# Optimization experiments

Measured on AMD Instinct MI355X. Metric: run time of the kernel, lower is better.

Reference implementation:

```python
import jax, jax.numpy as jnp
import numpy as np

B, S, N, C = 128, 512, 64, 1
F = N * C          # flattened feature dim = input_size * n_nodes
H = 512            # hidden_size


def _gru_imputer(x2d, m2d, Wih, Whh, bih, bhh, Wro, bro):
    """Unidirectional 1-step-ahead GRU imputer.
    x2d: [B,S,F] float, m2d: [B,S,F] bool.
    Returns (x_hat [B,S,F], h [B,S,H])."""
    dt = x2d.dtype
    h0 = jnp.zeros((x2d.shape[0], H), dtype=dt)
    xhat0 = h0 @ Wro.T + bro  # readout of initial state (== bro)

    def step(carry, inp):
        h, xhat = carry
        x_t, m_t = inp  # [B,F] float, [B,F] bool
        x_p = jnp.where(m_t, x_t, xhat)
        x_in = jnp.concatenate([x_p, m_t.astype(dt)], axis=-1)  # [B,2F]
        gi = x_in @ Wih.T + bih  # [B,3H]
        gh = h @ Whh.T + bhh     # [B,3H]
        ir, iz, inn = jnp.split(gi, 3, axis=-1)
        hr, hz, hn = jnp.split(gh, 3, axis=-1)
        r = jax.nn.sigmoid(ir + hr)
        z = jax.nn.sigmoid(iz + hz)
        n = jnp.tanh(inn + r * hn)
        h_new = (1.0 - z) * n + z * h
        xhat_new = h_new @ Wro.T + bro
        return (h_new, xhat_new), (h_new, xhat_new)

    xs = (jnp.swapaxes(x2d[:, :-1], 0, 1), jnp.swapaxes(m2d[:, :-1], 0, 1))
    _, (hs, xhats) = jax.lax.scan(step, (h0, xhat0), xs)
    hs = jnp.concatenate([h0[None], hs], axis=0)        # [S,B,H]
    xhats = jnp.concatenate([xhat0[None], xhats], axis=0)  # [S,B,F]
    return jnp.swapaxes(xhats, 0, 1), jnp.swapaxes(hs, 0, 1)


def setup_inputs() -> dict:
    key = jax.random.key(0)
    ks = jax.random.split(key, 16)
    s = 1.0 / np.sqrt(H)
    u = lambda k, shape: jax.random.uniform(k, shape, jnp.float32, -s, s)
    inp = {
        "x": jax.random.normal(ks[0], (B, S, N, C), jnp.float32),
        "mask": jax.random.randint(ks[1], (B, S, N, C), 0, 2).astype(bool),
        # forward-direction RNN params
        "Wih_f": u(ks[2], (3 * H, 2 * F)),
        "Whh_f": u(ks[3], (3 * H, H)),
        "bih_f": u(ks[4], (3 * H,)),
        "bhh_f": u(ks[5], (3 * H,)),
        "Wro_f": u(ks[6], (F, H)),
        "bro_f": u(ks[7], (F,)),
        # backward-direction RNN params
        "Wih_b": u(ks[8], (3 * H, 2 * F)),
        "Whh_b": u(ks[9], (3 * H, H)),
        "bih_b": u(ks[10], (3 * H,)),
        "bhh_b": u(ks[11], (3 * H,)),
        "Wro_b": u(ks[12], (F, H)),
        "bro_b": u(ks[13], (F,)),
        # final bidirectional readout
        "Wout": u(ks[14], (F, 2 * H)),
        "bout": u(ks[15], (F,)),
    }
    return inp


def reference(x, mask, Wih_f, Whh_f, bih_f, bhh_f, Wro_f, bro_f,
              Wih_b, Whh_b, bih_b, bhh_b, Wro_b, bro_b, Wout, bout):
    # rearrange 'b s n c -> b s (n c)'
    x2d = x.reshape(B, S, F)
    m2d = mask.reshape(B, S, F)

    xh_f, h_f = _gru_imputer(x2d, m2d, Wih_f, Whh_f, bih_f, bhh_f, Wro_f, bro_f)
    xh_b, h_b = _gru_imputer(x2d[:, ::-1], m2d[:, ::-1],
                             Wih_b, Whh_b, bih_b, bhh_b, Wro_b, bro_b)
    xh_b = xh_b[:, ::-1]
    h_b = h_b[:, ::-1]

    h = jnp.concatenate([h_f, h_b], axis=-1)  # [B,S,2H]; dropout p=0 -> identity
    x_hat = (h @ Wout.T + bout).reshape(B, S, N, C)
    return (x_hat, xh_f.reshape(B, S, N, C), xh_b.reshape(B, S, N, C))
```

## Files before the change

kernel.cpp:

```cpp
#include <hip/hip_runtime.h>

#define Bx 128
#define Sx 512
#define Fx 64
#define Hx 512
#define Xx 128

#define PARTB_OFF 0ull
#define H_OFF     ((size_t)Bx * Sx * Fx)
#define XHB_OFF   (H_OFF + (size_t)2 * 2 * Hx * Bx)
#define BAR_OFF   (XHB_OFF + (size_t)4 * 2 * Bx * Fx)
#define FLAG_OFF  (BAR_OFF + 4096)

#define LDSW_WHH   0
#define LDSW_XIN   26112
#define LDSW_WRO   (LDSW_XIN + 32 * 160)
#define LDSW_WOUT  (LDSW_WRO + 2 * 544)
#define LDSW_WROS  (LDSW_WOUT + 2 * 544)
#define LDSW_HX    (LDSW_WROS + 1088)
#define LDSW_TOTAL (LDSW_HX + 512 + 16)

struct BParams {
  const float* x; const void* mask;
  const float* Wih_f; const float* Whh_f; const float* bih_f; const float* bhh_f;
  const float* Wro_f; const float* bro_f;
  const float* Wih_b; const float* Whh_b; const float* bih_b; const float* bhh_b;
  const float* Wro_b; const float* bro_b;
  const float* Wout; const float* bout;
  float* out; float* ws;
};

__global__ void detect_kernel(const unsigned int* mask, float* ws) {
  int* bars = (int*)(ws + BAR_OFF);
  int* flag = (int*)(ws + FLAG_OFF);
  int t = threadIdx.x;
  for (int i = t; i < 4096; i += blockDim.x) bars[i] = 0;
  if (t == 0) *flag = 0;
  __syncthreads();
  unsigned int v = 0;
  for (int i = t; i < 4096; i += blockDim.x) v |= mask[i] & 0xFFFFFF00u;
  if (v) atomicOr(flag, 1);
}

__global__ void combine_kernel(float* out, const float* partb, const float* bout) {
  int i = blockIdx.x * blockDim.x + threadIdx.x;
  out[i] = out[i] + partb[i] + bout[i & 63];
}

__device__ __forceinline__ float sel8(const float* a, int idx) {
  float v = a[0];
#pragma unroll
  for (int i = 1; i < 8; ++i) v = (idx == i) ? a[i] : v;
  return v;
}

__device__ __forceinline__ void st_sys(float* p, float v) {
  __hip_atomic_store(p, v, __ATOMIC_RELAXED, __HIP_MEMORY_SCOPE_SYSTEM);
}
__device__ __forceinline__ void st_sys_i(int* p, int v) {
  __hip_atomic_store(p, v, __ATOMIC_RELAXED, __HIP_MEMORY_SCOPE_SYSTEM);
}

__device__ __forceinline__ void gbar(int* slots, int hs, int nbar) {
  __syncthreads();
  if (threadIdx.x < 64) {
    if (threadIdx.x == 0) st_sys_i(slots + hs * 16, nbar);
    const int* myslot = slots + (threadIdx.x & 31) * 16;
    for (;;) {
      int v = __hip_atomic_load(myslot, __ATOMIC_RELAXED, __HIP_MEMORY_SCOPE_AGENT);
      if (__all(v >= nbar)) break;
      __builtin_amdgcn_s_sleep(1);
    }
    asm volatile("buffer_inv\n\ts_waitcnt vmcnt(0)" ::: "memory");
  }
  __syncthreads();
}

#define GH_STEP(C, JOFF) {                                                   \
  const float* hr = hrd + (size_t)(j0 + jj + (JOFF)) * Bx + bA;              \
  float4 ha  = *(const float4*)(hr);                                         \
  float4 hbv = *(const float4*)(hr + 4);                                     \
  float s0 = w0.C, s1 = w1.C, s2 = w2.C;                                     \
  acc0[0]=fmaf(s0,ha.x,acc0[0]);  acc0[1]=fmaf(s0,ha.y,acc0[1]);             \
  acc0[2]=fmaf(s0,ha.z,acc0[2]);  acc0[3]=fmaf(s0,ha.w,acc0[3]);             \
  acc0[4]=fmaf(s0,hbv.x,acc0[4]); acc0[5]=fmaf(s0,hbv.y,acc0[5]);            \
  acc0[6]=fmaf(s0,hbv.z,acc0[6]); acc0[7]=fmaf(s0,hbv.w,acc0[7]);            \
  acc1[0]=fmaf(s1,ha.x,acc1[0]);  acc1[1]=fmaf(s1,ha.y,acc1[1]);             \
  acc1[2]=fmaf(s1,ha.z,acc1[2]);  acc1[3]=fmaf(s1,ha.w,acc1[3]);             \
  acc1[4]=fmaf(s1,hbv.x,acc1[4]); acc1[5]=fmaf(s1,hbv.y,acc1[5]);            \
  acc1[6]=fmaf(s1,hbv.z,acc1[6]); acc1[7]=fmaf(s1,hbv.w,acc1[7]);            \
  acc3[0]=fmaf(s2,ha.x,acc3[0]);  acc3[1]=fmaf(s2,ha.y,acc3[1]);             \
  acc3[2]=fmaf(s2,ha.z,acc3[2]);  acc3[3]=fmaf(s2,ha.w,acc3[3]);             \
  acc3[4]=fmaf(s2,hbv.x,acc3[4]); acc3[5]=fmaf(s2,hbv.y,acc3[5]);            \
  acc3[6]=fmaf(s2,hbv.z,acc3[6]); acc3[7]=fmaf(s2,hbv.w,acc3[7]); }

__global__ void __launch_bounds__(512, 2)
birnn_main(BParams p) {
  extern __shared__ float lds[];

  const int w   = blockIdx.x;
  const int g   = w & 7;
  const int dir = g >> 2;
  const int bg  = g & 3;
  const int hs  = w >> 3;
  const int b0  = bg * 32;
  const int u0  = hs * 16;
  const int f0  = hs * 2;
  const int tid = threadIdx.x;

  const float* Wih = dir ? p.Wih_b : p.Wih_f;
  const float* Whh = dir ? p.Whh_b : p.Whh_f;
  const float* bih = dir ? p.bih_b : p.bih_f;
  const float* bhh = dir ? p.bhh_b : p.bhh_f;
  const float* Wro = dir ? p.Wro_b : p.Wro_f;
  const float* bro = dir ? p.bro_b : p.bro_f;

  float* hbuf  = p.ws + H_OFF;
  float* xhb4  = p.ws + XHB_OFF;
  int*   slots = (int*)(p.ws + BAR_OFF) + g * 512;
  const int u8f = *(const int*)(p.ws + FLAG_OFF);
  const unsigned char* m8  = (const unsigned char*)p.mask;
  const int*           m32 = (const int*)p.mask;

  float* pout   = dir ? (p.ws + PARTB_OFF) : p.out;
  float* out_xh = p.out + (size_t)(1 + dir) * Bx * Sx * Fx;

  for (int idx = tid; idx < 3 * 16 * 512; idx += 512) {
    int g3 = idx >> 13; int rem = idx & 8191;
    int u = rem >> 9;   int j = rem & 511;
    lds[LDSW_WHH + ((g3 * 16 + u) * 8 + (j >> 6)) * 68 + (j & 63)] =
        Whh[(size_t)(g3 * 512 + u0 + u) * Hx + j];
  }
  for (int idx = tid; idx < 2 * 512; idx += 512) {
    int f = idx >> 9, j = idx & 511;
    lds[LDSW_WRO  + f * 544 + (j >> 6) * 68 + (j & 63)] = Wro[(size_t)(f0 + f) * Hx + j];
    lds[LDSW_WOUT + f * 544 + (j >> 6) * 68 + (j & 63)] =
        p.Wout[(size_t)(f0 + f) * (2 * Hx) + dir * Hx + j];
  }
  for (int idx = tid; idx < 64 * 16; idx += 512) {
    int f = idx >> 4, u = idx & 15;
    lds[LDSW_WROS + f * 17 + u] = Wro[(size_t)f * Hx + u0 + u];
  }

  if (hs == 0) {
    for (int idx = tid; idx < 32 * 512; idx += 512) {
      int u = idx >> 5, bo = idx & 31;
      st_sys(&hbuf[((size_t)(dir * 2 + 0) * Hx + u) * Bx + b0 + bo], 0.f);
    }
  }
  float bro_own = 0.f;
  if (tid < 64) {
    bro_own = bro[tid];
#pragma unroll
    for (int q = 0; q < 4; ++q)
      st_sys(&xhb4[(((size_t)q * 2 + dir) * Bx + (b0 + hs)) * Fx + tid], bro_own);
  }

  const int jq   = tid & 7;
  const int ulo  = (tid >> 3) & 7;
  const int wv   = tid >> 6;
  const int bsub = wv & 3;
  const int uhi  = wv >> 2;
  const int u    = uhi * 8 + ulo;
  const int bA   = b0 + bsub * 8;
  const int ru   = u0 + u;
  const int j0   = jq * 64;
  const int blo  = (tid >> 3) & 7;
  const int bB   = b0 + (wv & 3) * 8 + blo;
  const int fB   = wv >> 2;
  const int pf   = tid & 63;
  const int pbq  = tid >> 6;

  float4 wih0[4], wih1[4], wih2[4];
#pragma unroll
  for (int q = 0; q < 4; ++q) {
    wih0[q] = *(const float4*)(Wih + (size_t)(0 * 512 + ru) * Xx + jq * 16 + q * 4);
    wih1[q] = *(const float4*)(Wih + (size_t)(1 * 512 + ru) * Xx + jq * 16 + q * 4);
    wih2[q] = *(const float4*)(Wih + (size_t)(2 * 512 + ru) * Xx + jq * 16 + q * 4);
  }
  const float bs_r = bih[ru] + bhh[ru];
  const float bs_z = bih[512 + ru] + bhh[512 + ru];
  const float bs_i = bih[1024 + ru];
  const float bs_h = bhh[1024 + ru];

  const float* w0p = lds + LDSW_WHH + ((0 * 16 + u) * 8 + jq) * 68;
  const float* w1p = lds + LDSW_WHH + ((1 * 16 + u) * 8 + jq) * 68;
  const float* w2p = lds + LDSW_WHH + ((2 * 16 + u) * 8 + jq) * 68;

  float hprev_own = 0.f;

  int nbar = 1;
  gbar(slots, hs, nbar);

  for (int k = 1; k < Sx; ++k) {
    const int pp = k & 1, pr = pp ^ 1;
    const int t_in = dir ? (Sx - k) : (k - 1);
    const int rdq = (k - 1) & 3;
    const int adq = k & 3;
    const int inq = (k + 2) & 3;

    {
      int bl = tid >> 4, sub = tid & 15;
      int b = b0 + bl;
      float* xr = lds + LDSW_XIN + bl * 160 + (sub >> 1) * 20 + (sub & 1) * 8;
      float v[8];
      if (sub < 8) {
        size_t base = ((size_t)b * Sx + t_in) * Fx + sub * 8;
        float4 xa = *(const float4*)(p.x + base);
        float4 xb = *(const float4*)(p.x + base + 4);
        const float* xhp = xhb4 + (((size_t)rdq * 2 + dir) * Bx + b) * Fx + sub * 8;
        float4 ha  = *(const float4*)(xhp);
        float4 hb4 = *(const float4*)(xhp + 4);
        int mi[8];
        if (u8f) {
          unsigned long long mm = *(const unsigned long long*)(m8 + base);
#pragma unroll
          for (int j = 0; j < 8; ++j) mi[j] = (int)((mm >> (8 * j)) & 0xFF);
        } else {
          int4 ma = *(const int4*)(m32 + base);
          int4 mb = *(const int4*)(m32 + base + 4);
          mi[0] = ma.x; mi[1] = ma.y; mi[2] = ma.z; mi[3] = ma.w;
          mi[4] = mb.x; mi[5] = mb.y; mi[6] = mb.z; mi[7] = mb.w;
        }
        v[0] = mi[0] ? xa.x : ha.x;  v[1] = mi[1] ? xa.y : ha.y;
        v[2] = mi[2] ? xa.z : ha.z;  v[3] = mi[3] ? xa.w : ha.w;
        v[4] = mi[4] ? xb.x : hb4.x; v[5] = mi[5] ? xb.y : hb4.y;
        v[6] = mi[6] ? xb.z : hb4.z; v[7] = mi[7] ? xb.w : hb4.w;
      } else {
        size_t base = ((size_t)b * Sx + t_in) * Fx + (sub - 8) * 8;
        if (u8f) {
          unsigned long long mm = *(const unsigned long long*)(m8 + base);
#pragma unroll
          for (int j = 0; j < 8; ++j) v[j] = (float)((mm >> (8 * j)) & 0xFF);
        } else {
          int4 ma = *(const int4*)(m32 + base);
          int4 mb = *(const int4*)(m32 + base + 4);
          v[0] = (float)ma.x; v[1] = (float)ma.y; v[2] = (float)ma.z; v[3] = (float)ma.w;
          v[4] = (float)mb.x; v[5] = (float)mb.y; v[6] = (float)mb.z; v[7] = (float)mb.w;
        }
      }
      *(float4*)(xr)     = make_float4(v[0], v[1], v[2], v[3]);
      *(float4*)(xr + 4) = make_float4(v[4], v[5], v[6], v[7]);
    }
    if (tid < 64) {
      float v = xhb4[(((size_t)rdq * 2 + dir) * Bx + (b0 + hs)) * Fx + tid];
      st_sys(&out_xh[((size_t)(b0 + hs) * Sx + t_in) * Fx + tid], v);
    }
    {
      const float* hnw  = hbuf + (size_t)(dir * 2 + pr) * Hx * Bx;
      const float* wouL = lds + LDSW_WOUT + fB * 544 + jq * 68;
      const float* hcol = hnw + (size_t)j0 * Bx + bB;
      float ap = 0.f;
#pragma unroll 4
      for (int jj = 0; jj < 64; jj += 4) {
        float4 wp = *(const float4*)(wouL + jj);
        float h0 = hcol[(size_t)(jj + 0) * Bx];
        float h1 = hcol[(size_t)(jj + 1) * Bx];
        float h2 = hcol[(size_t)(jj + 2) * Bx];
        float h3 = hcol[(size_t)(jj + 3) * Bx];
        ap = fmaf(wp.x, h0, ap); ap = fmaf(wp.y, h1, ap);
        ap = fmaf(wp.z, h2, ap); ap = fmaf(wp.w, h3, ap);
      }
#pragma unroll
      for (int m = 1; m <= 4; m <<= 1) ap += __shfl_xor(ap, m);
      if (jq == 0)
        st_sys(&pout[((size_t)bB * Sx + t_in) * Fx + f0 + fB], ap);
    }
    __syncthreads();

    float acc0[8], acc1[8], acc2[8], acc3[8];
#pragma unroll
    for (int i = 0; i < 8; ++i) { acc0[i] = 0.f; acc1[i] = 0.f; acc2[i] = 0.f; acc3[i] = 0.f; }

    {
      const float* hrd = hbuf + (size_t)(dir * 2 + pr) * Hx * Bx;
#pragma unroll 2
      for (int jj = 0; jj < 64; jj += 4) {
        float4 w0 = *(const float4*)(w0p + jj);
        float4 w1 = *(const float4*)(w1p + jj);
        float4 w2 = *(const float4*)(w2p + jj);
        GH_STEP(x, 0)
        GH_STEP(y, 1)
        GH_STEP(z, 2)
        GH_STEP(w, 3)
      }
    }
    {
      const float* xinb = lds + LDSW_XIN;
#pragma unroll
      for (int q = 0; q < 4; ++q) {
        float4 w0 = wih0[q], w1 = wih1[q], w2 = wih2[q];
        int off = jq * 20 + q * 4;
#pragma unroll
        for (int bb = 0; bb < 8; ++bb) {
          float4 xv = *(const float4*)(xinb + (bsub * 8 + bb) * 160 + off);
          acc0[bb] = fmaf(w0.x, xv.x, acc0[bb]); acc0[bb] = fmaf(w0.y, xv.y, acc0[bb]);
          acc0[bb] = fmaf(w0.z, xv.z, acc0[bb]); acc0[bb] = fmaf(w0.w, xv.w, acc0[bb]);
          acc1[bb] = fmaf(w1.x, xv.x, acc1[bb]); acc1[bb] = fmaf(w1.y, xv.y, acc1[bb]);
          acc1[bb] = fmaf(w1.z, xv.z, acc1[bb]); acc1[bb] = fmaf(w1.w, xv.w, acc1[bb]);
          acc2[bb] = fmaf(w2.x, xv.x, acc2[bb]); acc2[bb] = fmaf(w2.y, xv.y, acc2[bb]);
          acc2[bb] = fmaf(w2.z, xv.z, acc2[bb]); acc2[bb] = fmaf(w2.w, xv.w, acc2[bb]);
        }
      }
    }
#pragma unroll
    for (int m = 1; m <= 4; m <<= 1) {
#pragma unroll
      for (int bb = 0; bb < 8; ++bb) {
        acc0[bb] += __shfl_xor(acc0[bb], m);
        acc1[bb] += __shfl_xor(acc1[bb], m);
        acc2[bb] += __shfl_xor(acc2[bb], m);
        acc3[bb] += __shfl_xor(acc3[bb], m);
      }
    }
    {
      int b = bA + jq;
      float sr  = sel8(acc0, jq);
      float sz  = sel8(acc1, jq);
      float sgi = sel8(acc2, jq);
      float sgh = sel8(acc3, jq);
      float r = 1.f / (1.f + __expf(-(sr + bs_r)));
      float z = 1.f / (1.f + __expf(-(sz + bs_z)));
      float n = tanhf(sgi + bs_i + r * (sgh + bs_h));
      float hn = (1.f - z) * n + z * hprev_own;
      hprev_own = hn;
      st_sys(&hbuf[((size_t)(dir * 2 + pp) * Hx + ru) * Bx + b], hn);
      lds[LDSW_HX + (bsub * 8 + jq) * 16 + u] = hn;
    }
    __syncthreads();

    {
      const float* wros = lds + LDSW_WROS + pf * 17;
      float* xq = xhb4 + (((size_t)adq * 2 + dir) * Bx + b0) * Fx;
#pragma unroll
      for (int i = 0; i < 4; ++i) {
        int bl = pbq * 4 + i;
        const float* hx = lds + LDSW_HX + bl * 16;
        float s = 0.f;
#pragma unroll
        for (int uu = 0; uu < 16; ++uu) s = fmaf(wros[uu], hx[uu], s);
        atomicAdd(xq + (size_t)bl * Fx + pf, s);
      }
    }
    if (tid < 64)
      st_sys(&xhb4[(((size_t)inq * 2 + dir) * Bx + (b0 + hs)) * Fx + tid], bro_own);

    ++nbar;
    gbar(slots, hs, nbar);
  }

  {
    const int ppE = (Sx - 1) & 1;
    const int tE  = dir ? 0 : (Sx - 1);
    const float* hnw  = hbuf + (size_t)(dir * 2 + ppE) * Hx * Bx;
    const float* wroL = lds + LDSW_WRO  + fB * 544 + jq * 68;
    const float* wouL = lds + LDSW_WOUT + fB * 544 + jq * 68;
    const float* hcol = hnw + (size_t)j0 * Bx + bB;
    float ax = 0.f, ap = 0.f;
#pragma unroll 4
    for (int jj = 0; jj < 64; jj += 4) {
      float4 wx = *(const float4*)(wroL + jj);
      float4 wp = *(const float4*)(wouL + jj);
      float h0 = hcol[(size_t)(jj + 0) * Bx];
      float h1 = hcol[(size_t)(jj + 1) * Bx];
      float h2 = hcol[(size_t)(jj + 2) * Bx];
      float h3 = hcol[(size_t)(jj + 3) * Bx];
      ax = fmaf(wx.x, h0, ax); ap = fmaf(wp.x, h0, ap);
      ax = fmaf(wx.y, h1, ax); ap = fmaf(wp.y, h1, ap);
      ax = fmaf(wx.z, h2, ax); ap = fmaf(wp.z, h2, ap);
      ax = fmaf(wx.w, h3, ax); ap = fmaf(wp.w, h3, ap);
    }
#pragma unroll
    for (int m = 1; m <= 4; m <<= 1) {
      ax += __shfl_xor(ax, m);
      ap += __shfl_xor(ap, m);
    }
    const int f = f0 + fB;
    if (jq == 0)
      st_sys(&out_xh[((size_t)bB * Sx + tE) * Fx + f], ax + bro[f]);
    else if (jq == 1)
      st_sys(&pout[((size_t)bB * Sx + tE) * Fx + f], ap);
  }
}

extern "C" void kernel_launch(void* const* d_in, const int* in_sizes, int n_in,
                              void* d_out, int out_size, void* d_ws, size_t ws_size,
                              hipStream_t stream) {
  (void)in_sizes; (void)n_in; (void)out_size; (void)ws_size;
  float* ws = (float*)d_ws;

  detect_kernel<<<1, 512, 0, stream>>>((const unsigned int*)d_in[1], ws);

  BParams p;
  p.x     = (const float*)d_in[0];  p.mask = d_in[1];
  p.Wih_f = (const float*)d_in[2];  p.Whh_f = (const float*)d_in[3];
  p.bih_f = (const float*)d_in[4];  p.bhh_f = (const float*)d_in[5];
  p.Wro_f = (const float*)d_in[6];  p.bro_f = (const float*)d_in[7];
  p.Wih_b = (const float*)d_in[8];  p.Whh_b = (const float*)d_in[9];
  p.bih_b = (const float*)d_in[10]; p.bhh_b = (const float*)d_in[11];
  p.Wro_b = (const float*)d_in[12]; p.bro_b = (const float*)d_in[13];
  p.Wout  = (const float*)d_in[14]; p.bout  = (const float*)d_in[15];
  p.out   = (float*)d_out;
  p.ws    = ws;

  hipFuncSetAttribute(reinterpret_cast<const void*>(birnn_main),
                      hipFuncAttributeMaxDynamicSharedMemorySize,
                      (int)(LDSW_TOTAL * sizeof(float)));
  void* args[] = { (void*)&p };
  hipLaunchCooperativeKernel(reinterpret_cast<void*>(birnn_main),
                             dim3(256), dim3(512), args,
                             (unsigned)(LDSW_TOTAL * sizeof(float)), stream);

  combine_kernel<<<dim3(Bx * Sx * Fx / 256), dim3(256), 0, stream>>>(
      (float*)d_out, ws + PARTB_OFF, (const float*)d_in[15]);
}
```

Measured before the change: 21.13 ms.

## Fuse output projection into per-step readout via atomic accumulation of hidden slices

The final Wout projection used to be a separate per-step pass that reread the whole previous hidden state from global memory. It is now computed from each block's local 16-unit hidden slice in LDS, alongside the xhat readout, and accumulated into the output with atomicAdd. A new init kernel zeroes the output and partial buffers first. This removes a global-memory reread and reduction from the critical step path, but adds many global atomics per step plus an extra zeroing pass.

```diff
diff --git a/kernel.cpp b/kernel.cpp
--- a/kernel.cpp
+++ b/kernel.cpp
@@ -15,9 +15,9 @@
 #define LDSW_WHH   0
 #define LDSW_XIN   26112
 #define LDSW_WRO   (LDSW_XIN + 32 * 160)
-#define LDSW_WOUT  (LDSW_WRO + 2 * 544)
-#define LDSW_WROS  (LDSW_WOUT + 2 * 544)
-#define LDSW_HX    (LDSW_WROS + 1088)
+#define LDSW_WROS  (LDSW_WRO + 2 * 544)
+#define LDSW_WOUTS (LDSW_WROS + 1088)
+#define LDSW_HX    (LDSW_WOUTS + 1088)
 #define LDSW_TOTAL (LDSW_HX + 512 + 16)
 
 struct BParams {
@@ -40,6 +40,15 @@
   unsigned int v = 0;
   for (int i = t; i < 4096; i += blockDim.x) v |= mask[i] & 0xFFFFFF00u;
   if (v) atomicOr(flag, 1);
+}
+
+__global__ void init_kernel(float* out, float* partb) {
+  size_t i = (size_t)blockIdx.x * blockDim.x + threadIdx.x;
+  const size_t n = (size_t)Bx * Sx * Fx / 4;
+  if (i < n) {
+    ((float4*)out)[i]   = make_float4(0.f, 0.f, 0.f, 0.f);
+    ((float4*)partb)[i] = make_float4(0.f, 0.f, 0.f, 0.f);
+  }
 }
 
 __global__ void combine_kernel(float* out, const float* partb, const float* bout) {
@@ -133,13 +142,12 @@
   }
   for (int idx = tid; idx < 2 * 512; idx += 512) {
     int f = idx >> 9, j = idx & 511;
-    lds[LDSW_WRO  + f * 544 + (j >> 6) * 68 + (j & 63)] = Wro[(size_t)(f0 + f) * Hx + j];
-    lds[LDSW_WOUT + f * 544 + (j >> 6) * 68 + (j & 63)] =
-        p.Wout[(size_t)(f0 + f) * (2 * Hx) + dir * Hx + j];
+    lds[LDSW_WRO + f * 544 + (j >> 6) * 68 + (j & 63)] = Wro[(size_t)(f0 + f) * Hx + j];
   }
   for (int idx = tid; idx < 64 * 16; idx += 512) {
     int f = idx >> 4, u = idx & 15;
-    lds[LDSW_WROS + f * 17 + u] = Wro[(size_t)f * Hx + u0 + u];
+    lds[LDSW_WROS  + f * 17 + u] = Wro[(size_t)f * Hx + u0 + u];
+    lds[LDSW_WOUTS + f * 17 + u] = p.Wout[(size_t)f * (2 * Hx) + dir * Hx + u0 + u];
   }
 
   if (hs == 0) {
@@ -195,6 +203,7 @@
   for (int k = 1; k < Sx; ++k) {
     const int pp = k & 1, pr = pp ^ 1;
     const int t_in = dir ? (Sx - k) : (k - 1);
+    const int T_k  = dir ? (Sx - 1 - k) : k;
     const int rdq = (k - 1) & 3;
     const int adq = k & 3;
     const int inq = (k + 2) & 3;
@@ -246,26 +255,6 @@
       float v = xhb4[(((size_t)rdq * 2 + dir) * Bx + (b0 + hs)) * Fx + tid];
       st_sys(&out_xh[((size_t)(b0 + hs) * Sx + t_in) * Fx + tid], v);
     }
-    {
-      const float* hnw  = hbuf + (size_t)(dir * 2 + pr) * Hx * Bx;
-      const float* wouL = lds + LDSW_WOUT + fB * 544 + jq * 68;
-      const float* hcol = hnw + (size_t)j0 * Bx + bB;
-      float ap = 0.f;
-#pragma unroll 4
-      for (int jj = 0; jj < 64; jj += 4) {
-        float4 wp = *(const float4*)(wouL + jj);
-        float h0 = hcol[(size_t)(jj + 0) * Bx];
-        float h1 = hcol[(size_t)(jj + 1) * Bx];
-        float h2 = hcol[(size_t)(jj + 2) * Bx];
-        float h3 = hcol[(size_t)(jj + 3) * Bx];
-        ap = fmaf(wp.x, h0, ap); ap = fmaf(wp.y, h1, ap);
-        ap = fmaf(wp.z, h2, ap); ap = fmaf(wp.w, h3, ap);
-      }
-#pragma unroll
-      for (int m = 1; m <= 4; m <<= 1) ap += __shfl_xor(ap, m);
-      if (jq == 0)
-        st_sys(&pout[((size_t)bB * Sx + t_in) * Fx + f0 + fB], ap);
-    }
     __syncthreads();
 
     float acc0[8], acc1[8], acc2[8], acc3[8];
@@ -330,16 +319,22 @@
     __syncthreads();
 
     {
-      const float* wros = lds + LDSW_WROS + pf * 17;
+      const float* wros = lds + LDSW_WROS  + pf * 17;
+      const float* wout = lds + LDSW_WOUTS + pf * 17;
       float* xq = xhb4 + (((size_t)adq * 2 + dir) * Bx + b0) * Fx;
 #pragma unroll
       for (int i = 0; i < 4; ++i) {
         int bl = pbq * 4 + i;
         const float* hx = lds + LDSW_HX + bl * 16;
-        float s = 0.f;
-#pragma unroll
-        for (int uu = 0; uu < 16; ++uu) s = fmaf(wros[uu], hx[uu], s);
+        float s = 0.f, s2 = 0.f;
+#pragma unroll
+        for (int uu = 0; uu < 16; ++uu) {
+          float hv = hx[uu];
+          s  = fmaf(wros[uu], hv, s);
+          s2 = fmaf(wout[uu], hv, s2);
+        }
         atomicAdd(xq + (size_t)bl * Fx + pf, s);
+        atomicAdd(pout + ((size_t)(b0 + bl) * Sx + T_k) * Fx + pf, s2);
       }
     }
     if (tid < 64)
@@ -353,33 +348,22 @@
     const int ppE = (Sx - 1) & 1;
     const int tE  = dir ? 0 : (Sx - 1);
     const float* hnw  = hbuf + (size_t)(dir * 2 + ppE) * Hx * Bx;
-    const float* wroL = lds + LDSW_WRO  + fB * 544 + jq * 68;
-    const float* wouL = lds + LDSW_WOUT + fB * 544 + jq * 68;
+    const float* wroL = lds + LDSW_WRO + fB * 544 + jq * 68;
     const float* hcol = hnw + (size_t)j0 * Bx + bB;
-    float ax = 0.f, ap = 0.f;
+    float ax = 0.f;
 #pragma unroll 4
     for (int jj = 0; jj < 64; jj += 4) {
       float4 wx = *(const float4*)(wroL + jj);
-      float4 wp = *(const float4*)(wouL + jj);
-      float h0 = hcol[(size_t)(jj + 0) * Bx];
-      float h1 = hcol[(size_t)(jj + 1) * Bx];
-      float h2 = hcol[(size_t)(jj + 2) * Bx];
-      float h3 = hcol[(size_t)(jj + 3) * Bx];
-      ax = fmaf(wx.x, h0, ax); ap = fmaf(wp.x, h0, ap);
-      ax = fmaf(wx.y, h1, ax); ap = fmaf(wp.y, h1, ap);
-      ax = fmaf(wx.z, h2, ax); ap = fmaf(wp.z, h2, ap);
-      ax = fmaf(wx.w, h3, ax); ap = fmaf(wp.w, h3, ap);
-    }
-#pragma unroll
-    for (int m = 1; m <= 4; m <<= 1) {
-      ax += __shfl_xor(ax, m);
-      ap += __shfl_xor(ap, m);
-    }
+      ax = fmaf(wx.x, hcol[(size_t)(jj + 0) * Bx], ax);
+      ax = fmaf(wx.y, hcol[(size_t)(jj + 1) * Bx], ax);
+      ax = fmaf(wx.z, hcol[(size_t)(jj + 2) * Bx], ax);
+      ax = fmaf(wx.w, hcol[(size_t)(jj + 3) * Bx], ax);
+    }
+#pragma unroll
+    for (int m = 1; m <= 4; m <<= 1) ax += __shfl_xor(ax, m);
     const int f = f0 + fB;
     if (jq == 0)
       st_sys(&out_xh[((size_t)bB * Sx + tE) * Fx + f], ax + bro[f]);
-    else if (jq == 1)
-      st_sys(&pout[((size_t)bB * Sx + tE) * Fx + f], ap);
   }
 }
 
@@ -390,6 +374,8 @@
   float* ws = (float*)d_ws;
 
   detect_kernel<<<1, 512, 0, stream>>>((const unsigned int*)d_in[1], ws);
+  init_kernel<<<(Bx * Sx * Fx / 4 + 255) / 256, 256, 0, stream>>>(
+      (float*)d_out, ws + PARTB_OFF);
 
   BParams p;
   p.x     = (const float*)d_in[0];  p.mask = d_in[1];
```

Measured after the change: 18.40 ms. 12.9% less time.
